# Kernel tuning notes

Hardware: AMD Instinct MI355X
Metric: run time of the kernel (lower is better)

Reference implementation:

```python
import jax, jax.numpy as jnp
import numpy as np

B, T, D, O, E = 4, 4096, 256, 256, 16


def setup_inputs() -> dict:
    key = jax.random.key(0)
    ks = jax.random.split(key, 5)
    s_in = 1.0 / np.sqrt(D)
    x = jax.random.normal(ks[0], (B, T, D), dtype=jnp.float32)
    We = jax.random.uniform(ks[1], (E, D, O), minval=-s_in, maxval=s_in, dtype=jnp.float32)
    be = jax.random.uniform(ks[2], (E, O), minval=-s_in, maxval=s_in, dtype=jnp.float32)
    Wg = jax.random.uniform(ks[3], (D, E), minval=-s_in, maxval=s_in, dtype=jnp.float32)
    bg = jax.random.uniform(ks[4], (E,), minval=-s_in, maxval=s_in, dtype=jnp.float32)
    return {"x": x, "We": We, "be": be, "Wg": Wg, "bg": bg}


def reference(x, We, be, Wg, bg):
    # gate: softmax over experts  [B,T,E]
    gate = jax.nn.softmax(jnp.einsum("btd,de->bte", x, Wg) + bg, axis=-1)
    # all experts: batched GEMM  [B,T,E,O]
    h = jax.nn.gelu(jnp.einsum("btd,edo->bteo", x, We) + be, approximate=False)
    # softmax-weighted sum over experts  [B,T,O]
    return jnp.einsum("bteo,bte->bto", h, gate)
```

## Files before the change

kernel.cpp:

```cpp
#include <hip/hip_runtime.h>
#include <stdint.h>

#define KD 256
#define NO 256
#define NE 16
#define BM 64
#define BN 128
#define XROW 264
#define GROW 68

typedef short bf16x8 __attribute__((ext_vector_type(8)));
typedef float f32x4 __attribute__((ext_vector_type(4)));

__device__ __forceinline__ unsigned short f2bf(float f) {
  uint32_t u = __float_as_uint(f);
  u += 0x7fffu + ((u >> 16) & 1u);
  return (unsigned short)(u >> 16);
}
__device__ __forceinline__ float bf2f(unsigned short h) {
  return __uint_as_float(((uint32_t)h) << 16);
}
__device__ __forceinline__ float gelu_f(float h) {
#if __has_builtin(__builtin_amdgcn_exp2f)
  float zn = h * fmaf(-0.10294817f, h * h, -2.3022077f);
  return h * __builtin_amdgcn_rcpf(1.0f + __builtin_amdgcn_exp2f(zn));
#else
  float z = h * fmaf(0.07135481627f, h * h, 1.5957691216f);
  return h * __builtin_amdgcn_rcpf(1.0f + __expf(-z));
#endif
}

__global__ void moe_prep(const float* __restrict__ We, unsigned short* __restrict__ Wf,
                         const float* __restrict__ Wg, unsigned short* __restrict__ Wgt)
{
  __shared__ float ts[256 * 17];
  const int tid = threadIdx.x;
  const int bid = blockIdx.x;
  if (bid < 256) {
    const int e = bid >> 4, ob = bid & 15;
    const float* src = We + (size_t)e * KD * NO + ob * 16;
    const int o = tid & 15, dg = tid >> 4;
#pragma unroll
    for (int p = 0; p < 16; ++p) {
      int d = p * 16 + dg;
      ts[d * 17 + o] = src[(size_t)d * NO + o];
    }
    __syncthreads();
    const int w = tid >> 6, l = tid & 63;
    const int q = l >> 4, ln = l & 15;
#pragma unroll
    for (int kk = 0; kk < 2; ++kk) {
      int kc = w + kk * 4;
      unsigned int pk[4];
#pragma unroll
      for (int h = 0; h < 4; ++h) {
        unsigned short lo = f2bf(ts[(kc * 32 + q * 8 + h * 2 + 0) * 17 + ln]);
        unsigned short hi = f2bf(ts[(kc * 32 + q * 8 + h * 2 + 1) * 17 + ln]);
        pk[h] = (unsigned int)lo | ((unsigned int)hi << 16);
      }
      uint4* dst = (uint4*)(Wf + ((((size_t)(e * 8 + kc) * 16 + ob) * 64) + l) * 8);
      *dst = make_uint4(pk[0], pk[1], pk[2], pk[3]);
    }
  } else {
    int d = tid;
    const float* wr = Wg + (size_t)d * NE;
#pragma unroll
    for (int e = 0; e < NE; ++e)
      Wgt[e * KD + d] = f2bf(wr[e]);
  }
}

__launch_bounds__(256, 2)
__global__ void moe_main(const float* __restrict__ x,
                         const uint4* __restrict__ Wf,
                         const unsigned short* __restrict__ Wgt,
                         const float* __restrict__ be,
                         const float* __restrict__ bg,
                         float* __restrict__ out)
{
  __shared__ __align__(16) unsigned short Xs[BM * XROW];
  __shared__ __align__(16) float gate_t[NE * GROW];
  __shared__ unsigned short be_h[NE * BN];

  const int tid = threadIdx.x;
  const int bid = blockIdx.x;
  const int half = bid & 1;
  const int n0 = half * BN;
  const int m0 = (bid >> 1) * BM;
  const int w = tid >> 6, lane = tid & 63;
  const int ln = lane & 15, quad = lane >> 4;
  const int eoff = __builtin_amdgcn_readfirstlane(((tid >> 6) * 4 + bid) & 15);

  const int voff = (half * 8 + w * 2) * 64 + lane;

  {
    const float4* xg = (const float4*)x + (size_t)m0 * (KD / 4);
#pragma unroll
    for (int p = 0; p < 16; ++p) {
      int idx = p * 256 + tid;
      int r = idx >> 6, c = idx & 63;
      float4 v = xg[r * (KD / 4) + c];
      uint32_t lo = (uint32_t)f2bf(v.x) | ((uint32_t)f2bf(v.y) << 16);
      uint32_t hi = (uint32_t)f2bf(v.z) | ((uint32_t)f2bf(v.w) << 16);
      *(uint2*)&Xs[r * XROW + c * 4] = make_uint2(lo, hi);
    }
  }
  uint4 b[4][2];
#pragma unroll
  for (int kc = 0; kc < 4; ++kc) {
    const uint4* p = Wf + ((size_t)eoff * 8 + kc) * 1024 + voff;
    b[kc][0] = p[0]; b[kc][1] = p[64];
  }
#pragma unroll
  for (int p = 0; p < 8; ++p) {
    int idx = p * 256 + tid;
    int e = idx >> 7, c = idx & 127;
    be_h[e * BN + c] = f2bf(be[e * NO + n0 + c]);
  }
  __syncthreads();

  bf16x8 a[4][8];
#pragma unroll
  for (int i = 0; i < 4; ++i)
#pragma unroll
    for (int kc = 0; kc < 8; ++kc)
      a[i][kc] = *(const bf16x8*)&Xs[(i * 16 + ln) * XROW + kc * 32 + quad * 8];

  {
    f32x4 g = {0.f, 0.f, 0.f, 0.f};
#pragma unroll
    for (int kc = 0; kc < 8; ++kc) {
      bf16x8 af = *(const bf16x8*)&Xs[(w * 16 + ln) * XROW + kc * 32 + quad * 8];
      bf16x8 wb = *(const bf16x8*)(Wgt + (size_t)ln * KD + kc * 32 + quad * 8);
      g = __builtin_amdgcn_mfma_f32_16x16x32_bf16(af, wb, g, 0, 0, 0);
    }
    float bgl = bg[ln];
#pragma unroll
    for (int r = 0; r < 4; ++r) {
      float v = g[r] + bgl;
      float mx = v;
#pragma unroll
      for (int msk = 1; msk < 16; msk <<= 1)
        mx = fmaxf(mx, __shfl_xor(mx, msk, 64));
      float ev = __expf(v - mx);
      float s = ev;
#pragma unroll
      for (int msk = 1; msk < 16; msk <<= 1)
        s += __shfl_xor(s, msk, 64);
      gate_t[ln * GROW + w * 16 + quad * 4 + r] = ev * __builtin_amdgcn_rcpf(s);
    }
  }
  __syncthreads();

  f32x4 acc[4][2], oacc[4][2];
#pragma unroll
  for (int i = 0; i < 4; ++i)
#pragma unroll
    for (int j = 0; j < 2; ++j) {
      acc[i][j] = (f32x4){0.f, 0.f, 0.f, 0.f};
      oacc[i][j] = (f32x4){0.f, 0.f, 0.f, 0.f};
    }

#pragma unroll 1
  for (int ei = 0; ei < NE; ++ei) {
    const int e  = (eoff + ei) & 15;
    const int en = (eoff + ei + 1) & 15;
    const uint4* bse = Wf + (size_t)e  * 8192 + voff;
    const uint4* bsn = Wf + (size_t)en * 8192 + voff;

#pragma unroll
    for (int kc = 0; kc < 8; ++kc) {
      uint4* bc = b[kc & 3];
#pragma unroll
      for (int i = 0; i < 4; ++i)
#pragma unroll
        for (int j = 0; j < 2; ++j)
          acc[i][j] = __builtin_amdgcn_mfma_f32_16x16x32_bf16(
              a[i][kc], *(const bf16x8*)&bc[j], acc[i][j], 0, 0, 0);
      if (kc < 4) {
        const uint4* p = bse + (kc + 4) * 1024;
        bc[0] = p[0]; bc[1] = p[64];
      } else if (ei < NE - 1) {
        const uint4* p = bsn + (kc - 4) * 1024;
        bc[0] = p[0]; bc[1] = p[64];
      }
    }
    {
      f32x4 gv[4];
#pragma unroll
      for (int i = 0; i < 4; ++i)
        gv[i] = *(const f32x4*)&gate_t[e * GROW + i * 16 + quad * 4];
      const float bb0 = bf2f(be_h[e * BN + w * 32 + ln]);
      const float bb1 = bf2f(be_h[e * BN + w * 32 + 16 + ln]);
#pragma unroll
      for (int i = 0; i < 4; ++i)
#pragma unroll
        for (int j = 0; j < 2; ++j)
#pragma unroll
          for (int r = 0; r < 4; ++r) {
            float hh = acc[i][j][r] + (j ? bb1 : bb0);
            oacc[i][j][r] = fmaf(gv[i][r], gelu_f(hh), oacc[i][j][r]);
            acc[i][j][r] = 0.f;
          }
    }
  }

#pragma unroll
  for (int i = 0; i < 4; ++i)
#pragma unroll
    for (int r = 0; r < 4; ++r) {
      int row = m0 + i * 16 + quad * 4 + r;
      float* orow = out + (size_t)row * NO + n0 + w * 32 + ln;
      orow[0]  = oacc[i][0][r];
      orow[16] = oacc[i][1][r];
    }
}

extern "C" void kernel_launch(void* const* d_in, const int* in_sizes, int n_in,
                              void* d_out, int out_size, void* d_ws, size_t ws_size,
                              hipStream_t stream) {
  const float* x  = (const float*)d_in[0];
  const float* We = (const float*)d_in[1];
  const float* be = (const float*)d_in[2];
  const float* Wg = (const float*)d_in[3];
  const float* bg = (const float*)d_in[4];
  float* out = (float*)d_out;
  unsigned short* Wf  = (unsigned short*)d_ws;
  unsigned short* Wgt = (unsigned short*)((char*)d_ws + (size_t)NE * NO * KD * 2);

  moe_prep<<<257, 256, 0, stream>>>(We, Wf, Wg, Wgt);
  moe_main<<<512, 256, 0, stream>>>(x, (const uint4*)Wf, Wgt, be, bg, out);
}
```

Before: 121.1 us.

## Split expert GEMM into two column halves with double-buffered weight registers

Restructures the per-expert loop so each wave computes one 16-column half at a time, with a short accumulator per row block and the GELU/gate epilogue run right after each half. Weight fragments are held in two 8-entry register buffers: one half's weights load while the other half computes, and the next expert's first-half weights are prefetched. The aim is to interleave the epilogue math with MFMA work and to shrink live accumulator registers. The cost is more weight registers (16 uint4 instead of 8), and the gate vector is now loaded twice per expert.

```diff
diff --git a/kernel.cpp b/kernel.cpp
--- a/kernel.cpp
+++ b/kernel.cpp
@@ -105,11 +105,11 @@
       *(uint2*)&Xs[r * XROW + c * 4] = make_uint2(lo, hi);
     }
   }
-  uint4 b[4][2];
-#pragma unroll
-  for (int kc = 0; kc < 4; ++kc) {
-    const uint4* p = Wf + ((size_t)eoff * 8 + kc) * 1024 + voff;
-    b[kc][0] = p[0]; b[kc][1] = p[64];
+  uint4 bbA[8], bbB[8];
+  {
+    const uint4* p0 = Wf + (size_t)eoff * 8192 + voff;
+#pragma unroll
+    for (int kc = 0; kc < 8; ++kc) bbA[kc] = p0[kc * 1024];
   }
 #pragma unroll
   for (int p = 0; p < 8; ++p) {
@@ -152,56 +152,54 @@
   }
   __syncthreads();
 
-  f32x4 acc[4][2], oacc[4][2];
+  f32x4 oacc[4][2];
 #pragma unroll
   for (int i = 0; i < 4; ++i)
 #pragma unroll
-    for (int j = 0; j < 2; ++j) {
-      acc[i][j] = (f32x4){0.f, 0.f, 0.f, 0.f};
+    for (int j = 0; j < 2; ++j)
       oacc[i][j] = (f32x4){0.f, 0.f, 0.f, 0.f};
-    }
 
 #pragma unroll 1
   for (int ei = 0; ei < NE; ++ei) {
     const int e  = (eoff + ei) & 15;
     const int en = (eoff + ei + 1) & 15;
-    const uint4* bse = Wf + (size_t)e  * 8192 + voff;
-    const uint4* bsn = Wf + (size_t)en * 8192 + voff;
-
-#pragma unroll
-    for (int kc = 0; kc < 8; ++kc) {
-      uint4* bc = b[kc & 3];
-#pragma unroll
-      for (int i = 0; i < 4; ++i)
-#pragma unroll
-        for (int j = 0; j < 2; ++j)
-          acc[i][j] = __builtin_amdgcn_mfma_f32_16x16x32_bf16(
-              a[i][kc], *(const bf16x8*)&bc[j], acc[i][j], 0, 0, 0);
-      if (kc < 4) {
-        const uint4* p = bse + (kc + 4) * 1024;
-        bc[0] = p[0]; bc[1] = p[64];
-      } else if (ei < NE - 1) {
-        const uint4* p = bsn + (kc - 4) * 1024;
-        bc[0] = p[0]; bc[1] = p[64];
+    const uint4* __restrict__ bse = Wf + (size_t)e  * 8192 + voff;
+    const uint4* __restrict__ bsn = Wf + (size_t)en * 8192 + voff;
+    const float bb0 = bf2f(be_h[e * BN + w * 32 + ln]);
+    const float bb1 = bf2f(be_h[e * BN + w * 32 + 16 + ln]);
+
+#pragma unroll
+    for (int kc = 0; kc < 8; ++kc) bbB[kc] = bse[kc * 1024 + 64];
+#pragma unroll
+    for (int i = 0; i < 4; ++i) {
+      f32x4 gvq = *(const f32x4*)&gate_t[e * GROW + i * 16 + quad * 4];
+      f32x4 acc = {0.f, 0.f, 0.f, 0.f};
+#pragma unroll
+      for (int kc = 0; kc < 8; ++kc)
+        acc = __builtin_amdgcn_mfma_f32_16x16x32_bf16(
+            a[i][kc], *(const bf16x8*)&bbA[kc], acc, 0, 0, 0);
+#pragma unroll
+      for (int r = 0; r < 4; ++r) {
+        float hh = acc[r] + bb0;
+        oacc[i][0][r] = fmaf(gvq[r], gelu_f(hh), oacc[i][0][r]);
       }
     }
-    {
-      f32x4 gv[4];
-#pragma unroll
-      for (int i = 0; i < 4; ++i)
-        gv[i] = *(const f32x4*)&gate_t[e * GROW + i * 16 + quad * 4];
-      const float bb0 = bf2f(be_h[e * BN + w * 32 + ln]);
-      const float bb1 = bf2f(be_h[e * BN + w * 32 + 16 + ln]);
-#pragma unroll
-      for (int i = 0; i < 4; ++i)
-#pragma unroll
-        for (int j = 0; j < 2; ++j)
-#pragma unroll
-          for (int r = 0; r < 4; ++r) {
-            float hh = acc[i][j][r] + (j ? bb1 : bb0);
-            oacc[i][j][r] = fmaf(gv[i][r], gelu_f(hh), oacc[i][j][r]);
-            acc[i][j][r] = 0.f;
-          }
+
+#pragma unroll
+    for (int kc = 0; kc < 8; ++kc) bbA[kc] = bsn[kc * 1024];
+#pragma unroll
+    for (int i = 0; i < 4; ++i) {
+      f32x4 gvq = *(const f32x4*)&gate_t[e * GROW + i * 16 + quad * 4];
+      f32x4 acc = {0.f, 0.f, 0.f, 0.f};
+#pragma unroll
+      for (int kc = 0; kc < 8; ++kc)
+        acc = __builtin_amdgcn_mfma_f32_16x16x32_bf16(
+            a[i][kc], *(const bf16x8*)&bbB[kc], acc, 0, 0, 0);
+#pragma unroll
+      for (int r = 0; r < 4; ++r) {
+        float hh = acc[r] + bb1;
+        oacc[i][1][r] = fmaf(gvq[r], gelu_f(hh), oacc[i][1][r]);
+      }
     }
   }
 
```

Result: slower. 124.8 us (+3.1%).

## Overlap GELU-gate epilogue of previous expert with next expert's MFMAs via LDS stash

Applied to the files above, without the earlier changes.

Restructures the expert loop so each expert's accumulators are stashed into a per-thread LDS buffer. The GELU and gate-weighted accumulation for the previous expert then runs between the two halves of the current expert's MFMA k-loop, letting VALU/transcendental work overlap matrix-core work instead of serialising after it. The epilogue math is also rewritten in packed two-wide float vectors to allow packed FMA/mul instructions. The cost is about 36 KB of extra LDS per block, which pushes total LDS close to the per-CU limit at two blocks per CU, plus an LDS store and reload of the accumulators on every expert.

```diff
diff --git a/kernel.cpp b/kernel.cpp
--- a/kernel.cpp
+++ b/kernel.cpp
@@ -8,9 +8,11 @@
 #define BN 128
 #define XROW 264
 #define GROW 68
+#define SROW 36
 
 typedef short bf16x8 __attribute__((ext_vector_type(8)));
 typedef float f32x4 __attribute__((ext_vector_type(4)));
+typedef float f32x2 __attribute__((ext_vector_type(2)));
 
 __device__ __forceinline__ unsigned short f2bf(float f) {
   uint32_t u = __float_as_uint(f);
@@ -20,14 +22,21 @@
 __device__ __forceinline__ float bf2f(unsigned short h) {
   return __uint_as_float(((uint32_t)h) << 16);
 }
-__device__ __forceinline__ float gelu_f(float h) {
-#if __has_builtin(__builtin_amdgcn_exp2f)
-  float zn = h * fmaf(-0.10294817f, h * h, -2.3022077f);
-  return h * __builtin_amdgcn_rcpf(1.0f + __builtin_amdgcn_exp2f(zn));
-#else
-  float z = h * fmaf(0.07135481627f, h * h, 1.5957691216f);
-  return h * __builtin_amdgcn_rcpf(1.0f + __expf(-z));
-#endif
+
+__device__ __forceinline__ void epi_pair(f32x2 h, f32x2 gv, f32x2& o) {
+  f32x2 t = h * h;
+  f32x2 s = __builtin_elementwise_fma(t, (f32x2){-0.10294817f, -0.10294817f},
+                                      (f32x2){-2.3022077f, -2.3022077f});
+  f32x2 zn = h * s;
+  f32x2 ev;
+  ev.x = __builtin_amdgcn_exp2f(zn.x);
+  ev.y = __builtin_amdgcn_exp2f(zn.y);
+  f32x2 den = ev + 1.0f;
+  f32x2 r;
+  r.x = __builtin_amdgcn_rcpf(den.x);
+  r.y = __builtin_amdgcn_rcpf(den.y);
+  f32x2 g = h * r;
+  o = __builtin_elementwise_fma(gv, g, o);
 }
 
 __global__ void moe_prep(const float* __restrict__ We, unsigned short* __restrict__ Wf,
@@ -81,6 +90,7 @@
   __shared__ __align__(16) unsigned short Xs[BM * XROW];
   __shared__ __align__(16) float gate_t[NE * GROW];
   __shared__ unsigned short be_h[NE * BN];
+  __shared__ __align__(16) float stash[256 * SROW];
 
   const int tid = threadIdx.x;
   const int bid = blockIdx.x;
@@ -152,22 +162,22 @@
   }
   __syncthreads();
 
-  f32x4 acc[4][2], oacc[4][2];
+  f32x4 acc[4][2];
+  f32x2 oacc[4][2][2];
 #pragma unroll
   for (int i = 0; i < 4; ++i)
 #pragma unroll
     for (int j = 0; j < 2; ++j) {
       acc[i][j] = (f32x4){0.f, 0.f, 0.f, 0.f};
-      oacc[i][j] = (f32x4){0.f, 0.f, 0.f, 0.f};
-    }
-
-#pragma unroll 1
-  for (int ei = 0; ei < NE; ++ei) {
-    const int e  = (eoff + ei) & 15;
-    const int en = (eoff + ei + 1) & 15;
-    const uint4* bse = Wf + (size_t)e  * 8192 + voff;
-    const uint4* bsn = Wf + (size_t)en * 8192 + voff;
-
+      oacc[i][j][0] = (f32x2){0.f, 0.f};
+      oacc[i][j][1] = (f32x2){0.f, 0.f};
+    }
+
+  float* const sp = &stash[0] + tid * SROW;
+
+  {
+    const uint4* __restrict__ bse = Wf + (size_t)eoff * 8192 + voff;
+    const uint4* __restrict__ bsn = Wf + (size_t)((eoff + 1) & 15) * 8192 + voff;
 #pragma unroll
     for (int kc = 0; kc < 8; ++kc) {
       uint4* bc = b[kc & 3];
@@ -177,43 +187,102 @@
         for (int j = 0; j < 2; ++j)
           acc[i][j] = __builtin_amdgcn_mfma_f32_16x16x32_bf16(
               a[i][kc], *(const bf16x8*)&bc[j], acc[i][j], 0, 0, 0);
-      if (kc < 4) {
-        const uint4* p = bse + (kc + 4) * 1024;
-        bc[0] = p[0]; bc[1] = p[64];
-      } else if (ei < NE - 1) {
-        const uint4* p = bsn + (kc - 4) * 1024;
-        bc[0] = p[0]; bc[1] = p[64];
-      }
-    }
+      const uint4* p = (kc < 4) ? (bse + (kc + 4) * 1024) : (bsn + (kc - 4) * 1024);
+      bc[0] = p[0]; bc[1] = p[64];
+    }
+  }
+
+#pragma unroll 1
+  for (int ei = 1; ei < NE; ++ei) {
+    const int e  = (eoff + ei) & 15;
+    const int en = (eoff + ei + 1) & 15;
+    const int ep = (eoff + ei - 1) & 15;
+    const uint4* __restrict__ bse = Wf + (size_t)e  * 8192 + voff;
+    const uint4* __restrict__ bsn = Wf + (size_t)en * 8192 + voff;
+
+#pragma unroll
+    for (int i = 0; i < 4; ++i)
+#pragma unroll
+      for (int j = 0; j < 2; ++j) {
+        *(f32x4*)&sp[(i * 2 + j) * 4] = acc[i][j];
+        acc[i][j] = (f32x4){0.f, 0.f, 0.f, 0.f};
+      }
+
+#pragma unroll
+    for (int kc = 0; kc < 4; ++kc) {
+      uint4* bc = b[kc];
+#pragma unroll
+      for (int i = 0; i < 4; ++i)
+#pragma unroll
+        for (int j = 0; j < 2; ++j)
+          acc[i][j] = __builtin_amdgcn_mfma_f32_16x16x32_bf16(
+              a[i][kc], *(const bf16x8*)&bc[j], acc[i][j], 0, 0, 0);
+      const uint4* p = bse + (kc + 4) * 1024;
+      bc[0] = p[0]; bc[1] = p[64];
+    }
+
     {
-      f32x4 gv[4];
+      const float bp0 = bf2f(be_h[ep * BN + w * 32 + ln]);
+      const float bp1 = bf2f(be_h[ep * BN + w * 32 + 16 + ln]);
+#pragma unroll
+      for (int i = 0; i < 4; ++i) {
+        const f32x4 gq = *(const f32x4*)&gate_t[ep * GROW + i * 16 + quad * 4];
+#pragma unroll
+        for (int j = 0; j < 2; ++j) {
+          const f32x4 sv = *(const f32x4*)&sp[(i * 2 + j) * 4];
+          const float bb = j ? bp1 : bp0;
+          f32x2 h0 = {sv[0] + bb, sv[1] + bb};
+          f32x2 h1 = {sv[2] + bb, sv[3] + bb};
+          epi_pair(h0, (f32x2){gq[0], gq[1]}, oacc[i][j][0]);
+          epi_pair(h1, (f32x2){gq[2], gq[3]}, oacc[i][j][1]);
+        }
+      }
+    }
+
+#pragma unroll
+    for (int kc = 4; kc < 8; ++kc) {
+      uint4* bc = b[kc & 3];
 #pragma unroll
       for (int i = 0; i < 4; ++i)
-        gv[i] = *(const f32x4*)&gate_t[e * GROW + i * 16 + quad * 4];
-      const float bb0 = bf2f(be_h[e * BN + w * 32 + ln]);
-      const float bb1 = bf2f(be_h[e * BN + w * 32 + 16 + ln]);
-#pragma unroll
-      for (int i = 0; i < 4; ++i)
 #pragma unroll
         for (int j = 0; j < 2; ++j)
-#pragma unroll
-          for (int r = 0; r < 4; ++r) {
-            float hh = acc[i][j][r] + (j ? bb1 : bb0);
-            oacc[i][j][r] = fmaf(gv[i][r], gelu_f(hh), oacc[i][j][r]);
-            acc[i][j][r] = 0.f;
-          }
+          acc[i][j] = __builtin_amdgcn_mfma_f32_16x16x32_bf16(
+              a[i][kc], *(const bf16x8*)&bc[j], acc[i][j], 0, 0, 0);
+      const uint4* p = bsn + (kc - 4) * 1024;
+      bc[0] = p[0]; bc[1] = p[64];
+    }
+  }
+
+  {
+    const int ep = (eoff + NE - 1) & 15;
+    const float bp0 = bf2f(be_h[ep * BN + w * 32 + ln]);
+    const float bp1 = bf2f(be_h[ep * BN + w * 32 + 16 + ln]);
+#pragma unroll
+    for (int i = 0; i < 4; ++i) {
+      const f32x4 gq = *(const f32x4*)&gate_t[ep * GROW + i * 16 + quad * 4];
+#pragma unroll
+      for (int j = 0; j < 2; ++j) {
+        const f32x4 sv = acc[i][j];
+        const float bb = j ? bp1 : bp0;
+        f32x2 h0 = {sv[0] + bb, sv[1] + bb};
+        f32x2 h1 = {sv[2] + bb, sv[3] + bb};
+        epi_pair(h0, (f32x2){gq[0], gq[1]}, oacc[i][j][0]);
+        epi_pair(h1, (f32x2){gq[2], gq[3]}, oacc[i][j][1]);
+      }
     }
   }
 
 #pragma unroll
   for (int i = 0; i < 4; ++i)
 #pragma unroll
-    for (int r = 0; r < 4; ++r) {
-      int row = m0 + i * 16 + quad * 4 + r;
-      float* orow = out + (size_t)row * NO + n0 + w * 32 + ln;
-      orow[0]  = oacc[i][0][r];
-      orow[16] = oacc[i][1][r];
-    }
+    for (int rr = 0; rr < 2; ++rr)
+#pragma unroll
+      for (int c = 0; c < 2; ++c) {
+        int row = m0 + i * 16 + quad * 4 + rr * 2 + c;
+        float* orow = out + (size_t)row * NO + n0 + w * 32 + ln;
+        orow[0]  = oacc[i][0][rr][c];
+        orow[16] = oacc[i][1][rr][c];
+      }
 }
 
 extern "C" void kernel_launch(void* const* d_in, const int* in_sizes, int n_in,
```

After: 129.7 us. 1.07x slower.

## Stream A fragments from LDS and prefetch a full expert's weights into registers

Applied to the files above, without the earlier changes.

The kernel stops holding all 32 X fragments in registers. It copies them into an MFMA-ordered LDS buffer and double-buffers per-k-step loads from it. The freed registers hold all 8 k-chunks of the B weights, so the next expert's weights are prefetched a whole expert ahead instead of half an expert. This trades LDS reads and about 32KB of extra shared memory per block, which may hurt occupancy, for longer global-load latency hiding.

```diff
diff --git a/kernel.cpp b/kernel.cpp
--- a/kernel.cpp
+++ b/kernel.cpp
@@ -79,6 +79,7 @@
                          float* __restrict__ out)
 {
   __shared__ __align__(16) unsigned short Xs[BM * XROW];
+  __shared__ __align__(16) uint4 Af4[BM * KD / 8];
   __shared__ __align__(16) float gate_t[NE * GROW];
   __shared__ unsigned short be_h[NE * BN];
 
@@ -93,6 +94,13 @@
 
   const int voff = (half * 8 + w * 2) * 64 + lane;
 
+  uint4 b[8][2];
+#pragma unroll
+  for (int kc = 0; kc < 8; ++kc) {
+    const uint4* p = Wf + (size_t)eoff * 8192 + kc * 1024 + voff;
+    b[kc][0] = p[0]; b[kc][1] = p[64];
+  }
+
   {
     const float4* xg = (const float4*)x + (size_t)m0 * (KD / 4);
 #pragma unroll
@@ -105,12 +113,6 @@
       *(uint2*)&Xs[r * XROW + c * 4] = make_uint2(lo, hi);
     }
   }
-  uint4 b[4][2];
-#pragma unroll
-  for (int kc = 0; kc < 4; ++kc) {
-    const uint4* p = Wf + ((size_t)eoff * 8 + kc) * 1024 + voff;
-    b[kc][0] = p[0]; b[kc][1] = p[64];
-  }
 #pragma unroll
   for (int p = 0; p < 8; ++p) {
     int idx = p * 256 + tid;
@@ -119,12 +121,14 @@
   }
   __syncthreads();
 
-  bf16x8 a[4][8];
-#pragma unroll
-  for (int i = 0; i < 4; ++i)
-#pragma unroll
-    for (int kc = 0; kc < 8; ++kc)
-      a[i][kc] = *(const bf16x8*)&Xs[(i * 16 + ln) * XROW + kc * 32 + quad * 8];
+#pragma unroll
+  for (int kk = 0; kk < 2; ++kk) {
+    const int kc = w * 2 + kk;
+#pragma unroll
+    for (int i = 0; i < 4; ++i)
+      Af4[(i * 8 + kc) * 64 + lane] =
+          *(const uint4*)&Xs[(i * 16 + ln) * XROW + kc * 32 + quad * 8];
+  }
 
   {
     f32x4 g = {0.f, 0.f, 0.f, 0.f};
@@ -161,30 +165,39 @@
       oacc[i][j] = (f32x4){0.f, 0.f, 0.f, 0.f};
     }
 
+  bf16x8 a0[4], a1[4];
+#pragma unroll
+  for (int i = 0; i < 4; ++i)
+    a0[i] = *(const bf16x8*)&Af4[(i * 8 + 0) * 64 + lane];
+
 #pragma unroll 1
   for (int ei = 0; ei < NE; ++ei) {
     const int e  = (eoff + ei) & 15;
     const int en = (eoff + ei + 1) & 15;
-    const uint4* bse = Wf + (size_t)e  * 8192 + voff;
-    const uint4* bsn = Wf + (size_t)en * 8192 + voff;
+    const uint4* __restrict__ bsn = Wf + (size_t)en * 8192 + voff;
+
+    asm volatile("" ::: "memory");
 
 #pragma unroll
     for (int kc = 0; kc < 8; ++kc) {
-      uint4* bc = b[kc & 3];
+      bf16x8* acur = (kc & 1) ? a1 : a0;
+      bf16x8* anx  = (kc & 1) ? a0 : a1;
+      const int kn = (kc + 1) & 7;
+#pragma unroll
+      for (int i = 0; i < 4; ++i)
+        anx[i] = *(const bf16x8*)&Af4[(i * 8 + kn) * 64 + lane];
 #pragma unroll
       for (int i = 0; i < 4; ++i)
 #pragma unroll
         for (int j = 0; j < 2; ++j)
           acc[i][j] = __builtin_amdgcn_mfma_f32_16x16x32_bf16(
-              a[i][kc], *(const bf16x8*)&bc[j], acc[i][j], 0, 0, 0);
-      if (kc < 4) {
-        const uint4* p = bse + (kc + 4) * 1024;
-        bc[0] = p[0]; bc[1] = p[64];
-      } else if (ei < NE - 1) {
-        const uint4* p = bsn + (kc - 4) * 1024;
-        bc[0] = p[0]; bc[1] = p[64];
+              acur[i], *(const bf16x8*)&b[kc][j], acc[i][j], 0, 0, 0);
+      if (ei < NE - 1) {
+        const uint4* p = bsn + kc * 1024;
+        b[kc][0] = p[0]; b[kc][1] = p[64];
       }
     }
+
     {
       f32x4 gv[4];
 #pragma unroll
```

Measured after the change: 122.6 us. About the same (+1.2%).
